# Kernel optimization log

Hardware: AMD Instinct MI355X
Metric: run time of the kernel (lower is better)

Reference implementation:

```python
import jax, jax.numpy as jnp
import numpy as np

DIM = 256
CTX_DIM = 768
GROUPS = 8
EPS = 1e-5


def setup_inputs() -> dict:
    key = jax.random.key(0)
    ks = jax.random.split(key, 16)
    B, C, H, W, L = 16, DIM, 64, 64, 77
    s_conv = 1.0 / np.sqrt(C * 9)
    s_q = 1.0 / np.sqrt(C)
    s_kv = 1.0 / np.sqrt(CTX_DIM)
    return {
        "x": jax.random.normal(ks[0], (B, C, H, W), jnp.float32),
        "context": jax.random.normal(ks[1], (B, L, CTX_DIM), jnp.float32),
        "conv_w": jax.random.uniform(ks[2], (C, C, 3, 3), jnp.float32, -s_conv, s_conv),
        "conv_b": jax.random.uniform(ks[3], (C,), jnp.float32, -s_conv, s_conv),
        "gn_w": jnp.ones((C,), jnp.float32),
        "gn_b": jnp.zeros((C,), jnp.float32),
        "wq": jax.random.uniform(ks[4], (C, C), jnp.float32, -s_q, s_q),
        "bq": jax.random.uniform(ks[5], (C,), jnp.float32, -s_q, s_q),
        "wk": jax.random.uniform(ks[6], (C, CTX_DIM), jnp.float32, -s_kv, s_kv),
        "bk": jax.random.uniform(ks[7], (C,), jnp.float32, -s_kv, s_kv),
        "wv": jax.random.uniform(ks[8], (C, CTX_DIM), jnp.float32, -s_kv, s_kv),
        "bv": jax.random.uniform(ks[9], (C,), jnp.float32, -s_kv, s_kv),
        "wo": jax.random.uniform(ks[10], (C, C), jnp.float32, -s_q, s_q),
        "bo": jax.random.uniform(ks[11], (C,), jnp.float32, -s_q, s_q),
    }


def _group_norm(h, gn_w, gn_b):
    B, C, H, W = h.shape
    g = h.reshape(B, GROUPS, C // GROUPS, H, W)
    mean = g.mean(axis=(2, 3, 4), keepdims=True)
    var = g.var(axis=(2, 3, 4), keepdims=True)
    g = (g - mean) * jax.lax.rsqrt(var + EPS)
    h = g.reshape(B, C, H, W)
    return h * gn_w[None, :, None, None] + gn_b[None, :, None, None]


def reference(x, context, conv_w, conv_b, gn_w, gn_b, wq, bq, wk, bk, wv, bv, wo, bo):
    B, C, H, W = x.shape
    # conv 3x3, padding=1 (NCHW, OIHW)
    h = jax.lax.conv_general_dilated(
        x, conv_w, window_strides=(1, 1), padding=((1, 1), (1, 1)),
        dimension_numbers=("NCHW", "OIHW", "NCHW"))
    h = h + conv_b[None, :, None, None]
    h = jax.nn.silu(_group_norm(h, gn_w, gn_b))
    # flatten spatial -> tokens: [B, HW, C]
    hf = h.reshape(B, C, H * W).transpose(0, 2, 1)
    q = hf @ wq.T + bq                     # [B, HW, C]
    k = context @ wk.T + bk                # [B, L, C]
    v = context @ wv.T + bv                # [B, L, C]
    scale = 1.0 / jnp.sqrt(jnp.asarray(C, q.dtype))
    att = jax.nn.softmax(jnp.einsum("bqc,bkc->bqk", q, k) * scale, axis=-1)
    o = jnp.einsum("bqk,bkc->bqc", att, v) @ wo.T + bo
    h_att = o.transpose(0, 2, 1).reshape(B, C, H, W)
    return x + h_att
```

## Files before the change

kernel.cpp:

```cpp
#include <hip/hip_runtime.h>
#include <stdint.h>

#define B_  16
#define C_  256
#define HW_ 4096
#define Hp  66
#define PP  4356
#define EPS_ 1e-5f

typedef unsigned short u16;
typedef unsigned int   u32;
typedef __attribute__((ext_vector_type(4))) float  f32x4;
typedef __attribute__((ext_vector_type(8))) __bf16 bf16x8;
typedef __attribute__((ext_vector_type(8))) u16    u16x8;

__device__ __forceinline__ float bf2f(u16 u){ u32 x = ((u32)u)<<16; float f; __builtin_memcpy(&f,&x,4); return f; }
__device__ __forceinline__ u16 f2bf(float f){ u32 x; __builtin_memcpy(&x,&f,4); u32 r = x + 0x7fffu + ((x>>16)&1u); return (u16)(r>>16); }

__device__ __forceinline__ void g2l16(const void* g, void* l){
  __builtin_amdgcn_global_load_lds((__attribute__((address_space(1))) void*)(void*)g,
                                   (__attribute__((address_space(3))) void*)l, 16, 0, 0);
}
__device__ __forceinline__ bf16x8 ldfrag(const u16* p){
  u16x8 r = *(const u16x8*)p;
  return __builtin_bit_cast(bf16x8, r);
}

__global__ __launch_bounds__(256) void k_prep(const float* __restrict__ x, u16* __restrict__ xpT,
    const float* __restrict__ conv_w, const float* __restrict__ wq, const float* __restrict__ wo,
    const float* __restrict__ wk, const float* __restrict__ wv, const float* __restrict__ ctx,
    u16* __restrict__ wBt, u16* __restrict__ wqB, u16* __restrict__ woB,
    u16* __restrict__ wkvB, u16* __restrict__ ctxB, float* __restrict__ stats){
  __shared__ float Lt[64*65];
  int bid = blockIdx.x; int tid = threadIdx.x;
  if(bid >= 1056){
    int i = (bid-1056)*256 + tid;
    if(i < 589824){ int co = i/2304, k = i - co*2304; int t = k>>8, ci = k&255;
      wBt[i] = f2bf(conv_w[(co*256+ci)*9 + t]); return; }
    i -= 589824;
    if(i < 65536){ wqB[i] = f2bf(wq[i]); return; } i -= 65536;
    if(i < 65536){ woB[i] = f2bf(wo[i]); return; } i -= 65536;
    if(i < 196608){ wkvB[i] = f2bf(wk[i]); return; } i -= 196608;
    if(i < 196608){ wkvB[196608+i] = f2bf(wv[i]); return; } i -= 196608;
    if(i < 946176){ ctxB[i] = f2bf(ctx[i]); return; } i -= 946176;
    if(i < 512){ stats[i] = 0.f; }
    return;
  }
  int b = bid/66, hh = bid - b*66;
  u16* rowbase = xpT + (size_t)(b*PP + hh*Hp)*C_;
  if(hh==0 || hh==65){
    u32* p = (u32*)rowbase;
    for(int i=tid;i<66*C_/2;i+=256) p[i]=0u;
    return;
  }
  if(tid<128) ((u32*)rowbase)[tid]=0u;
  else ((u32*)(rowbase + 65*C_))[tid-128]=0u;
  int h = hh-1;
  for(int cc=0; cc<4; cc++){
    int c0=cc*64;
    int ci = tid>>2, w0 = (tid&3)*16;
    const float* xs = x + ((size_t)(b*C_ + c0+ci)*HW_) + h*64 + w0;
    for(int j=0;j<4;j++){
      float4 v = *(const float4*)(xs + j*4);
      Lt[ci*65 + w0 + j*4 + 0] = v.x;
      Lt[ci*65 + w0 + j*4 + 1] = v.y;
      Lt[ci*65 + w0 + j*4 + 2] = v.z;
      Lt[ci*65 + w0 + j*4 + 3] = v.w;
    }
    __syncthreads();
    int w = tid>>2, cj = (tid&3)*16;
    union { u16 u[16]; uint4 v[2]; } outu;
    for(int j=0;j<16;j++) outu.u[j] = f2bf(Lt[(cj+j)*65 + w]);
    uint4* dst = (uint4*)(rowbase + (size_t)(w+1)*C_ + c0 + cj);
    dst[0]=outu.v[0]; dst[1]=outu.v[1];
    __syncthreads();
  }
}

__global__ __launch_bounds__(256, 2) void k_conv(const u16* __restrict__ xpT, const u16* __restrict__ wBt,
    const float* __restrict__ conv_b, u16* __restrict__ h, float* __restrict__ stats){
  __shared__ u16 As[264*32];
  __shared__ u16 Bs[256*32];
  int bid = blockIdx.x;
  int b = bid >> 5, hp = bid & 31;
  int tid = threadIdx.x;
  int w = tid>>6, lane = tid&63, ln = lane&15, qd = lane>>4;
  int wm = w&1, wn = w>>1;
  const u16* Abase = xpT + (size_t)(b*PP + hp*132)*C_;
  f32x4 acc[4][8] = {};
  int hr_[4], wp_[4];
  #pragma unroll
  for(int mf=0;mf<4;mf++){ int p = wm*64 + mf*16 + ln; hr_[mf] = p>>6; wp_[mf] = p&63; }

  for(int ci=0; ci<8; ci++){
    int ci0 = ci*32;
    #pragma unroll
    for(int r=0;r<5;r++){
      int c = r*256 + tid;
      if(c < 1056){
        int ipix = c>>2, atom = c&3;
        g2l16(Abase + (size_t)ipix*C_ + ci0 + atom*8, &As[c*8]);
      }
    }
    for(int t=0;t<9;t++){
      int dy = (t*11)>>5, dx = t - dy*3;
      #pragma unroll
      for(int r=0;r<4;r++){
        int c = r*256 + tid;
        int co = c>>2, atom = c&3;
        g2l16(wBt + (size_t)co*2304 + t*256 + ci0 + atom*8, &Bs[c*8]);
      }
      __syncthreads();
      bf16x8 af[4], bfv[8];
      #pragma unroll
      for(int mf=0;mf<4;mf++){
        int ipix = (hr_[mf]+dy)*66 + wp_[mf] + dx;
        af[mf] = ldfrag(&As[ipix*32 + qd*8]);
      }
      #pragma unroll
      for(int nf=0;nf<8;nf++) bfv[nf] = ldfrag(&Bs[(wn*128+nf*16+ln)*32 + qd*8]);
      #pragma unroll
      for(int mf=0;mf<4;mf++)
        #pragma unroll
        for(int nf=0;nf<8;nf++)
          acc[mf][nf] = __builtin_amdgcn_mfma_f32_16x16x32_bf16(af[mf], bfv[nf], acc[mf][nf], 0,0,0);
      __syncthreads();
    }
  }
  float s[4]={0,0,0,0}, q[4]={0,0,0,0};
  int p0 = hp*128;
  for(int nf=0;nf<8;nf++){
    int n = wn*128 + nf*16 + ln;
    float bias = conv_b[n];
    for(int mf=0;mf<4;mf++){
      for(int r=0;r<4;r++){
        int p = wm*64 + mf*16 + qd*4 + r;
        float v = acc[mf][nf][r] + bias;
        h[((size_t)(b*HW_ + p0 + p))*C_ + n] = f2bf(v);
        s[nf>>1]+=v; q[nf>>1]+=v*v;
      }
    }
  }
  for(int off=32;off>=1;off>>=1){
    #pragma unroll
    for(int g=0;g<4;g++){ s[g]+=__shfl_down(s[g],off,64); q[g]+=__shfl_down(q[g],off,64); }
  }
  if(lane==0){
    #pragma unroll
    for(int g=0;g<4;g++){
      atomicAdd(&stats[(b*8 + wn*4 + g)*2+0], s[g]);
      atomicAdd(&stats[(b*8 + wn*4 + g)*2+1], q[g]);
    }
  }
}

__global__ __launch_bounds__(256, 2) void k_qgn(const u16* __restrict__ hbuf, const u16* __restrict__ wqB,
    const float* __restrict__ stats, const float* __restrict__ gnw, const float* __restrict__ gnb,
    const float* __restrict__ bq, u16* __restrict__ qb){
  __shared__ u16 As[128*32];
  __shared__ u16 Bs[256*32];
  int mt = blockIdx.x;
  int b = mt >> 5;
  int tid = threadIdx.x;
  int w = tid>>6, lane = tid&63, ln = lane&15, qd = lane>>4;
  int wm = w&1, wn = w>>1;
  int pr = tid>>1, half = tid&1;
  const u16* hsrc = hbuf + ((size_t)(mt*128+pr))*256 + half*16;
  f32x4 acc[4][8] = {};
  uint4 ra0, ra1, rb0, rb1;
  ra0 = *(const uint4*)(hsrc);
  ra1 = *(const uint4*)(hsrc + 8);
  for(int kt=0; kt<8; kt++){
    float sm = stats[(b*8+kt)*2], qm = stats[(b*8+kt)*2+1];
    float mean = sm*(1.f/131072.f);
    float rstd = rsqrtf(qm*(1.f/131072.f) - mean*mean + EPS_);
    int c0 = kt*32 + half*16;
    float4 gw0 = *(const float4*)(gnw+c0), gw1 = *(const float4*)(gnw+c0+4);
    float4 gw2 = *(const float4*)(gnw+c0+8), gw3 = *(const float4*)(gnw+c0+12);
    float4 gb0 = *(const float4*)(gnb+c0), gb1 = *(const float4*)(gnb+c0+4);
    float4 gb2 = *(const float4*)(gnb+c0+8), gb3 = *(const float4*)(gnb+c0+12);
    float gwv[16] = {gw0.x,gw0.y,gw0.z,gw0.w, gw1.x,gw1.y,gw1.z,gw1.w,
                     gw2.x,gw2.y,gw2.z,gw2.w, gw3.x,gw3.y,gw3.z,gw3.w};
    float gbv[16] = {gb0.x,gb0.y,gb0.z,gb0.w, gb1.x,gb1.y,gb1.z,gb1.w,
                     gb2.x,gb2.y,gb2.z,gb2.w, gb3.x,gb3.y,gb3.z,gb3.w};
    u16 inu[16];
    ((uint4*)inu)[0] = ra0; ((uint4*)inu)[1] = ra1;
    u16 outu[16];
    #pragma unroll
    for(int j=0;j<16;j++){
      float v = bf2f(inu[j]);
      v = (v-mean)*rstd*gwv[j] + gbv[j];
      float s = v/(1.f+__expf(-v));
      outu[j] = f2bf(s);
    }
    u16* adst = &As[pr*32 + half*16];
    ((uint4*)adst)[0] = ((uint4*)outu)[0];
    ((uint4*)adst)[1] = ((uint4*)outu)[1];
    #pragma unroll
    for(int r=0;r<4;r++){
      int c = r*256 + tid;
      int co = c>>2, atom = c&3;
      g2l16(wqB + (size_t)co*256 + kt*32 + atom*8, &Bs[c*8]);
    }
    if(kt<7){
      rb0 = *(const uint4*)(hsrc + (kt+1)*32);
      rb1 = *(const uint4*)(hsrc + (kt+1)*32 + 8);
    }
    __syncthreads();
    bf16x8 af[4], bfv[8];
    #pragma unroll
    for(int mf=0;mf<4;mf++) af[mf] = ldfrag(&As[(wm*64+mf*16+ln)*32 + qd*8]);
    #pragma unroll
    for(int nf=0;nf<8;nf++) bfv[nf] = ldfrag(&Bs[(wn*128+nf*16+ln)*32 + qd*8]);
    #pragma unroll
    for(int mf=0;mf<4;mf++)
      #pragma unroll
      for(int nf=0;nf<8;nf++)
        acc[mf][nf] = __builtin_amdgcn_mfma_f32_16x16x32_bf16(af[mf], bfv[nf], acc[mf][nf], 0,0,0);
    __syncthreads();
    ra0 = rb0; ra1 = rb1;
  }
  for(int nf=0;nf<8;nf++){
    int n = wn*128 + nf*16 + ln;
    float bias = bq[n];
    for(int mf=0;mf<4;mf++){
      for(int r=0;r<4;r++){
        int ml = wm*64 + mf*16 + qd*4 + r;
        qb[((size_t)(mt*128+ml))*256 + n] = f2bf(acc[mf][nf][r]+bias);
      }
    }
  }
}

__global__ __launch_bounds__(256) void k_kvproj(const u16* __restrict__ ctxB, const u16* __restrict__ wkvB,
    const float* __restrict__ bk, const float* __restrict__ bv,
    u16* __restrict__ kb, u16* __restrict__ vT){
  __shared__ u16 As[64*128];
  __shared__ u16 Bs[64*128];
  int bid = blockIdx.x;
  int nt = bid & 7, mt = bid >> 3;
  int n0 = nt*64, m0 = mt*64;
  int tid=threadIdx.x, w=tid>>6, lane=tid&63, ln=lane&15, qd=lane>>4;
  int wm = w&1, wn = w>>1;
  f32x4 acc[2][2]={};
  for(int kt=0;kt<6;kt++){
    #pragma unroll
    for(int r=0;r<4;r++){
      int c = r*256 + tid;
      int row = c>>4, atom = c&15;
      g2l16(ctxB + ((size_t)(m0+row)*768 + kt*128 + atom*8), &As[c*8]);
      g2l16(wkvB + ((size_t)(n0+row)*768 + kt*128 + atom*8), &Bs[c*8]);
    }
    __syncthreads();
    #pragma unroll
    for(int kk=0;kk<4;kk++){
      bf16x8 af[2], bfv[2];
      #pragma unroll
      for(int mf=0;mf<2;mf++) af[mf]=ldfrag(&As[(wm*32+mf*16+ln)*128 + kk*32 + qd*8]);
      #pragma unroll
      for(int nf=0;nf<2;nf++) bfv[nf]=ldfrag(&Bs[(wn*32+nf*16+ln)*128 + kk*32 + qd*8]);
      #pragma unroll
      for(int mf=0;mf<2;mf++)
        #pragma unroll
        for(int nf=0;nf<2;nf++)
          acc[mf][nf]=__builtin_amdgcn_mfma_f32_16x16x32_bf16(af[mf],bfv[nf],acc[mf][nf],0,0,0);
    }
    __syncthreads();
  }
  for(int mf=0;mf<2;mf++) for(int nf=0;nf<2;nf++){
    int ng = n0 + wn*32 + nf*16 + ln;
    float bias = ng<256 ? bk[ng] : bv[ng-256];
    for(int r=0;r<4;r++){
      int mg = m0 + wm*32 + mf*16 + qd*4 + r;
      if(mg<1232){
        float v=acc[mf][nf][r]+bias;
        int bb=mg/77, l=mg-bb*77;
        if(ng<256) kb[((size_t)(bb*77+l))*256+ng]=f2bf(v);
        else vT[((size_t)(bb*256+(ng-256)))*96 + l]=f2bf(v);
      }
    }
  }
}

__global__ __launch_bounds__(256) void k_attn(const u16* __restrict__ qg, const u16* __restrict__ kb,
    const u16* __restrict__ vT, u16* __restrict__ ob){
  __shared__ u16 Qs[4096];
  __shared__ u16 KVs[4096];
  __shared__ u16 Sb[128*88];
  __shared__ u16 Pb[128*104];
  __shared__ float invr[128];
  int bid=blockIdx.x; int b=bid>>5, qt=bid&31; int p0=qt*128;
  int tid=threadIdx.x, w=tid>>6, lane=tid&63, ln=lane&15, qd=lane>>4;
  int srow=tid>>2, koff=(tid&3)*8;
  f32x4 Sa[2][5]={};
  for(int kt=0;kt<8;kt++){
    for(int j=0;j<2;j++){
      int m=srow+j*64;
      g2l16(qg + ((size_t)(b*HW_+p0+m)*256 + kt*32+koff), &Qs[(size_t)tid*8+j*2048]);
    }
    for(int j=0;j<2;j++){
      int cja = tid + j*256;
      if(cja < 320){
        int l = cja>>2, ko2=(cja&3)*8;
        g2l16(kb + ((size_t)(b*77+l)*256 + kt*32+ko2), &KVs[(size_t)cja*8]);
      }
    }
    __syncthreads();
    bf16x8 af[2], bfv[5];
    for(int mf=0;mf<2;mf++) af[mf]=ldfrag(&Qs[(w*32+mf*16+ln)*32+qd*8]);
    for(int nf=0;nf<5;nf++) bfv[nf]=ldfrag(&KVs[(nf*16+ln)*32+qd*8]);
    for(int mf=0;mf<2;mf++) for(int nf=0;nf<5;nf++)
      Sa[mf][nf]=__builtin_amdgcn_mfma_f32_16x16x32_bf16(af[mf],bfv[nf],Sa[mf][nf],0,0,0);
    __syncthreads();
  }
  for(int mf=0;mf<2;mf++) for(int nf=0;nf<5;nf++) for(int r=0;r<4;r++){
    int ml=w*32+mf*16+qd*4+r, nl=nf*16+ln;
    Sb[ml*88+nl]=f2bf(Sa[mf][nf][r]*0.0625f);
  }
  __syncthreads();
  if(tid<128){
    u16* srp = &Sb[tid*88];
    srp[77]=0xFF80u; srp[78]=0xFF80u; srp[79]=0xFF80u;
    float mx=-1e30f;
    #pragma unroll
    for(int c8=0;c8<10;c8++){
      u16x8 v = *(const u16x8*)(srp + c8*8);
      #pragma unroll
      for(int j=0;j<8;j++) mx = fmaxf(mx, bf2f(v[j]));
    }
    u16* prow = &Pb[tid*104];
    float sum=0.f;
    #pragma unroll
    for(int c8=0;c8<10;c8++){
      u16x8 v = *(const u16x8*)(srp + c8*8);
      u16x8 o;
      #pragma unroll
      for(int j=0;j<8;j++){ float e=__expf(bf2f(v[j])-mx); sum+=e; o[j]=f2bf(e); }
      *(u16x8*)(prow + c8*8) = o;
    }
    #pragma unroll
    for(int j=80;j<96;j++) prow[j]=0;
    invr[tid] = 1.f/sum;
  }
  __syncthreads();
  for(int nh=0;nh<2;nh++){
    f32x4 Oa[2][8]={};
    for(int kt2=0;kt2<3;kt2++){
      for(int j=0;j<2;j++){
        int chunk=tid+j*256;
        int co=chunk>>2, ko2=(chunk&3)*8;
        g2l16(vT + ((size_t)(b*256+nh*128+co)*96 + kt2*32+ko2), &KVs[(size_t)chunk*8]);
      }
      __syncthreads();
      bf16x8 af[2], bfv[8];
      for(int mf=0;mf<2;mf++) af[mf]=ldfrag(&Pb[(w*32+mf*16+ln)*104 + kt2*32+qd*8]);
      for(int nf=0;nf<8;nf++) bfv[nf]=ldfrag(&KVs[(nf*16+ln)*32+qd*8]);
      for(int mf=0;mf<2;mf++) for(int nf=0;nf<8;nf++)
        Oa[mf][nf]=__builtin_amdgcn_mfma_f32_16x16x32_bf16(af[mf],bfv[nf],Oa[mf][nf],0,0,0);
      __syncthreads();
    }
    for(int mf=0;mf<2;mf++){
      #pragma unroll
      for(int r=0;r<4;r++){
        int ml=w*32+mf*16+qd*4+r;
        float inv = invr[ml];
        for(int nf=0;nf<8;nf++){
          int nl=nh*128+nf*16+ln;
          ob[((size_t)(b*HW_+p0+ml))*256+nl]=f2bf(Oa[mf][nf][r]*inv);
        }
      }
    }
  }
}

__global__ __launch_bounds__(256) void k_oproj(const u16* __restrict__ ob, const u16* __restrict__ woB,
    const float* __restrict__ bo, const float* __restrict__ x, float* __restrict__ outp){
  __shared__ u16 As[128*32];
  __shared__ u16 Bs[128*32];
  int bid=blockIdx.x;
  int b=bid>>6; int rr=bid&63; int cm=rr>>5, pt=rr&31;
  int c0=cm*128, p0=pt*128;
  int tid=threadIdx.x, w=tid>>6, lane=tid&63, ln=lane&15, qd=lane>>4, wm=w>>1, wn=w&1;
  int srow=tid>>2, koff=(tid&3)*8;
  f32x4 acc[4][4]={};
  for(int kt=0;kt<8;kt++){
    for(int j=0;j<2;j++){
      int m=srow+j*64;
      g2l16(woB + ((size_t)(c0+m)*256 + kt*32+koff),        &As[(size_t)tid*8+j*2048]);
      g2l16(ob  + ((size_t)(b*HW_+p0+m)*256 + kt*32+koff),  &Bs[(size_t)tid*8+j*2048]);
    }
    __syncthreads();
    bf16x8 af[4], bfv[4];
    for(int mf=0;mf<4;mf++) af[mf]=ldfrag(&As[(wm*64+mf*16+ln)*32+qd*8]);
    for(int nf=0;nf<4;nf++) bfv[nf]=ldfrag(&Bs[(wn*64+nf*16+ln)*32+qd*8]);
    for(int mf=0;mf<4;mf++) for(int nf=0;nf<4;nf++)
      acc[mf][nf]=__builtin_amdgcn_mfma_f32_16x16x32_bf16(af[mf],bfv[nf],acc[mf][nf],0,0,0);
    __syncthreads();
  }
  for(int mf=0;mf<4;mf++) for(int r=0;r<4;r++){
    int cl=c0+wm*64+mf*16+qd*4+r;
    float bias=bo[cl];
    for(int nf=0;nf<4;nf++){
      int pl=p0+wn*64+nf*16+ln;
      size_t idx=((size_t)(b*C_+cl))*HW_+pl;
      outp[idx]=x[idx]+acc[mf][nf][r]+bias;
    }
  }
}

extern "C" void kernel_launch(void* const* d_in, const int* in_sizes, int n_in,
                              void* d_out, int out_size, void* d_ws, size_t ws_size,
                              hipStream_t stream){
  const float* x      = (const float*)d_in[0];
  const float* ctx    = (const float*)d_in[1];
  const float* conv_w = (const float*)d_in[2];
  const float* conv_b = (const float*)d_in[3];
  const float* gnw    = (const float*)d_in[4];
  const float* gnb    = (const float*)d_in[5];
  const float* wq     = (const float*)d_in[6];
  const float* bq     = (const float*)d_in[7];
  const float* wk     = (const float*)d_in[8];
  const float* bk     = (const float*)d_in[9];
  const float* wv     = (const float*)d_in[10];
  const float* bv     = (const float*)d_in[11];
  const float* wo     = (const float*)d_in[12];
  const float* bo     = (const float*)d_in[13];
  char* ws = (char*)d_ws;
  u16* xpT  = (u16*)(ws + 0);
  u16* wBt  = (u16*)(ws + 35684352);
  u16* wqB  = (u16*)(ws + 36864000);
  u16* wkvB = (u16*)(ws + 36995072);
  u16* woB  = (u16*)(ws + 37781504);
  u16* ctxB = (u16*)(ws + 37912576);
  u16* hbuf = (u16*)(ws + 39804928);
  u16* kbv  = (u16*)(ws + 73359360);
  u16* vT   = (u16*)(ws + 73990144);
  u16* obuf = (u16*)(ws + 74776576);
  float* stats = (float*)(ws + 108331008);
  u16* qb = xpT;
  float* outp = (float*)d_out;

  k_prep  <<<9106, 256, 0, stream>>>(x, xpT, conv_w, wq, wo, wk, wv, ctx, wBt, wqB, woB, wkvB, ctxB, stats);
  k_conv  <<<512,  256, 0, stream>>>(xpT, wBt, conv_b, hbuf, stats);
  k_qgn   <<<512,  256, 0, stream>>>(hbuf, wqB, stats, gnw, gnb, bq, qb);
  k_kvproj<<<160,  256, 0, stream>>>(ctxB, wkvB, bk, bv, kbv, vT);
  k_attn  <<<512,  256, 0, stream>>>(qb, kbv, vT, obuf);
  k_oproj <<<1024, 256, 0, stream>>>(obuf, woB, bo, x, outp);
}
```

Baseline: 384.5 us.

## Double-buffer conv LDS tiles and re-layout inputs into channel-atom planes

The conv kernel now double-buffers both the activation and weight tiles in LDS, prefetching the next tap's weights and the next channel chunk's activations while the MFMAs for the current step run. This drops one barrier per step. The prep kernel writes the padded input and conv weights in a planar layout grouped by 8-channel atoms, so each 16-byte load and LDS fragment read is contiguous. This avoids strided 256-channel rows and likely LDS bank conflicts. In exchange, LDS use doubles (about 66KB per block), which may limit occupancy to fewer than 2 blocks per CU.

```diff
diff --git a/kernel.cpp b/kernel.cpp
--- a/kernel.cpp
+++ b/kernel.cpp
@@ -35,8 +35,12 @@
   int bid = blockIdx.x; int tid = threadIdx.x;
   if(bid >= 1056){
     int i = (bid-1056)*256 + tid;
-    if(i < 589824){ int co = i/2304, k = i - co*2304; int t = k>>8, ci = k&255;
-      wBt[i] = f2bf(conv_w[(co*256+ci)*9 + t]); return; }
+    if(i < 589824){
+      int j = i&7, co = (i>>3)&255, atom = (i>>11)&3, g = i>>13;
+      int t = g%9, cic = g/9;
+      int ciF = cic*32 + atom*8 + j;
+      wBt[i] = f2bf(conv_w[(co*256+ciF)*9 + t]); return;
+    }
     i -= 589824;
     if(i < 65536){ wqB[i] = f2bf(wq[i]); return; } i -= 65536;
     if(i < 65536){ woB[i] = f2bf(wo[i]); return; } i -= 65536;
@@ -47,14 +51,19 @@
     return;
   }
   int b = bid/66, hh = bid - b*66;
-  u16* rowbase = xpT + (size_t)(b*PP + hh*Hp)*C_;
   if(hh==0 || hh==65){
-    u32* p = (u32*)rowbase;
-    for(int i=tid;i<66*C_/2;i+=256) p[i]=0u;
+    for(int i=tid;i<32*264;i+=256){
+      int pl = i/264, off = i - pl*264;
+      u32* p = (u32*)(xpT + ((size_t)(b*32+pl)*PP + (size_t)hh*Hp)*8);
+      p[off] = 0u;
+    }
     return;
   }
-  if(tid<128) ((u32*)rowbase)[tid]=0u;
-  else ((u32*)(rowbase + 65*C_))[tid-128]=0u;
+  {
+    int pl = tid>>3, q = tid&7;
+    size_t base = ((size_t)(b*32+pl)*PP + (size_t)hh*Hp + (q>=4?65:0))*8;
+    ((u32*)(xpT + base))[q&3] = 0u;
+  }
   int h = hh-1;
   for(int cc=0; cc<4; cc++){
     int c0=cc*64;
@@ -71,60 +80,80 @@
     int w = tid>>2, cj = (tid&3)*16;
     union { u16 u[16]; uint4 v[2]; } outu;
     for(int j=0;j<16;j++) outu.u[j] = f2bf(Lt[(cj+j)*65 + w]);
-    uint4* dst = (uint4*)(rowbase + (size_t)(w+1)*C_ + c0 + cj);
-    dst[0]=outu.v[0]; dst[1]=outu.v[1];
+    int chan = c0 + cj;
+    int cic = chan>>5, at0 = (chan>>3)&3;
+    u16* dst = xpT + (((size_t)(b*8+cic)*4 + at0)*PP + (size_t)hh*Hp + w + 1)*8;
+    *(uint4*)dst = outu.v[0];
+    *(uint4*)(dst + (size_t)PP*8) = outu.v[1];
     __syncthreads();
   }
 }
 
 __global__ __launch_bounds__(256, 2) void k_conv(const u16* __restrict__ xpT, const u16* __restrict__ wBt,
     const float* __restrict__ conv_b, u16* __restrict__ h, float* __restrict__ stats){
-  __shared__ u16 As[264*32];
-  __shared__ u16 Bs[256*32];
+  __shared__ u16 As[2][264*32];
+  __shared__ u16 Bs[2][256*32];
   int bid = blockIdx.x;
   int b = bid >> 5, hp = bid & 31;
   int tid = threadIdx.x;
   int w = tid>>6, lane = tid&63, ln = lane&15, qd = lane>>4;
   int wm = w&1, wn = w>>1;
-  const u16* Abase = xpT + (size_t)(b*PP + hp*132)*C_;
   f32x4 acc[4][8] = {};
   int hr_[4], wp_[4];
   #pragma unroll
   for(int mf=0;mf<4;mf++){ int p = wm*64 + mf*16 + ln; hr_[mf] = p>>6; wp_[mf] = p&63; }
 
+  #pragma unroll
+  for(int r=0;r<5;r++){
+    int c = r*256 + tid;
+    if(c < 1056){
+      int atom = c/264, ipix = c - atom*264;
+      g2l16(xpT + (((size_t)(b*8+0)*4 + atom)*PP + hp*132 + ipix)*8, &As[0][c*8]);
+    }
+  }
+  #pragma unroll
+  for(int r=0;r<4;r++){
+    int c = r*256 + tid;
+    g2l16(wBt + (size_t)c*8, &Bs[0][c*8]);
+  }
+  __syncthreads();
+
+  int cb = 0;
   for(int ci=0; ci<8; ci++){
-    int ci0 = ci*32;
-    #pragma unroll
-    for(int r=0;r<5;r++){
-      int c = r*256 + tid;
-      if(c < 1056){
-        int ipix = c>>2, atom = c&3;
-        g2l16(Abase + (size_t)ipix*C_ + ci0 + atom*8, &As[c*8]);
-      }
-    }
+    int ca = ci&1;
     for(int t=0;t<9;t++){
+      int tn = t+1, cin = ci;
+      if(tn==9){ tn=0; cin=ci+1; }
+      if(cin < 8){
+        #pragma unroll
+        for(int r=0;r<4;r++){
+          int c = r*256 + tid;
+          g2l16(wBt + ((size_t)(cin*9+tn)*1024 + c)*8, &Bs[cb^1][c*8]);
+        }
+      }
+      if(t<5 && ci<7){
+        int c = t*256 + tid;
+        if(c < 1056){
+          int atom = c/264, ipix = c - atom*264;
+          g2l16(xpT + (((size_t)(b*8+ci+1)*4 + atom)*PP + hp*132 + ipix)*8, &As[ca^1][c*8]);
+        }
+      }
       int dy = (t*11)>>5, dx = t - dy*3;
-      #pragma unroll
-      for(int r=0;r<4;r++){
-        int c = r*256 + tid;
-        int co = c>>2, atom = c&3;
-        g2l16(wBt + (size_t)co*2304 + t*256 + ci0 + atom*8, &Bs[c*8]);
-      }
-      __syncthreads();
       bf16x8 af[4], bfv[8];
       #pragma unroll
       for(int mf=0;mf<4;mf++){
         int ipix = (hr_[mf]+dy)*66 + wp_[mf] + dx;
-        af[mf] = ldfrag(&As[ipix*32 + qd*8]);
-      }
-      #pragma unroll
-      for(int nf=0;nf<8;nf++) bfv[nf] = ldfrag(&Bs[(wn*128+nf*16+ln)*32 + qd*8]);
+        af[mf] = ldfrag(&As[ca][(qd*264 + ipix)*8]);
+      }
+      #pragma unroll
+      for(int nf=0;nf<8;nf++) bfv[nf] = ldfrag(&Bs[cb][(qd*256 + wn*128+nf*16+ln)*8]);
       #pragma unroll
       for(int mf=0;mf<4;mf++)
         #pragma unroll
         for(int nf=0;nf<8;nf++)
           acc[mf][nf] = __builtin_amdgcn_mfma_f32_16x16x32_bf16(af[mf], bfv[nf], acc[mf][nf], 0,0,0);
       __syncthreads();
+      cb ^= 1;
     }
   }
   float s[4]={0,0,0,0}, q[4]={0,0,0,0};
```

New measurement: 389.5 us. No clear change (+1.3%).
